# Kernel tuning notes

Hardware: AMD Instinct MI355X
Metric: run time of the kernel (lower is better)

Reference implementation:

```python
import jax, jax.numpy as jnp
import numpy as np

N_TOKENS = 50257  # vocab size (init kwarg)


def setup_inputs() -> dict:
    key = jax.random.key(0)
    # [batch, seq] int token ids in [0, N_TOKENS)
    inputs = jax.random.randint(key, (1024, 512), 0, N_TOKENS, dtype=jnp.int32)
    return {"inputs": inputs}


def reference(inputs) -> jnp.ndarray:
    # Faithful math: sum_j one_hot(inputs[b, j], N_TOKENS) -> token count histogram,
    # then drop token id 0 (padding). Implemented as a scatter-add instead of
    # materializing the [B, S, V] one-hot tensor.
    B, S = inputs.shape
    rows = jnp.arange(B, dtype=jnp.int32)[:, None]  # [B, 1] broadcast against [B, S]
    counts = jnp.zeros((B, N_TOKENS), dtype=jnp.float32)
    counts = counts.at[rows, inputs].add(jnp.float32(1.0))  # [B, V]
    return counts[:, 1:]  # drop token id 0, matches [:, 1:] in the original
```

## Files before the change

kernel.cpp:

```cpp
#include <hip/hip_runtime.h>


#define BATCH 1024
#define SEQ 512
#define VOCAB 50257
#define OUT_COLS (VOCAB - 1)
#define CHUNK 4096
#define NCHUNK 13
#define BLOCK 256

#define LDS_BAR()                                              \
    do {                                                       \
        asm volatile("s_waitcnt lgkmcnt(0)" ::: "memory");     \
        __builtin_amdgcn_s_barrier();                          \
        asm volatile("" ::: "memory");                         \
    } while (0)

__global__ __launch_bounds__(BLOCK) void bow_persistent_kernel(
    const int* __restrict__ tokens, float* __restrict__ out) {
    __shared__ unsigned int hist[CHUNK];

    const int t = threadIdx.x;
    const int b = blockIdx.x >> 1;
    const int h = blockIdx.x & 1;
    const int cbeg = h ? 7 : 0;
    const int cend = h ? NCHUNK : 7;

    const uint4 z4 = make_uint4(0u, 0u, 0u, 0u);
    #pragma unroll
    for (int k = 0; k < 4; ++k)
        *(uint4*)&hist[t * 4 + k * (BLOCK * 4)] = z4;

    const int2 tk = ((const int2*)(tokens + (size_t)b * SEQ))[t];
    const unsigned int cx = (unsigned int)(tk.x - 1);
    const unsigned int cy = (unsigned int)(tk.y - 1);

    LDS_BAR();

    for (int c = cbeg; c < cend; ++c) {
        const unsigned int c0 = (unsigned int)c * CHUNK;

        unsigned int r;
        r = cx - c0;
        if (r < CHUNK) atomicAdd(&hist[r], 1u);
        r = cy - c0;
        if (r < CHUNK) atomicAdd(&hist[r], 1u);

        LDS_BAR();

        uint4 hreg[4];
        #pragma unroll
        for (int k = 0; k < 4; ++k)
            hreg[k] = *(const uint4*)&hist[t * 4 + k * (BLOCK * 4)];
        #pragma unroll
        for (int k = 0; k < 4; ++k)
            *(uint4*)&hist[t * 4 + k * (BLOCK * 4)] = z4;

        LDS_BAR();

        float* orow = out + (size_t)b * OUT_COLS + c0;
        if (c0 + CHUNK <= (unsigned int)OUT_COLS) {
            #pragma unroll
            for (int k = 0; k < 4; ++k) {
                float4 v = make_float4((float)hreg[k].x, (float)hreg[k].y,
                                       (float)hreg[k].z, (float)hreg[k].w);
                *(float4*)(orow + t * 4 + k * (BLOCK * 4)) = v;
            }
        } else {
            const int ncols = OUT_COLS - (int)c0;
            #pragma unroll
            for (int k = 0; k < 4; ++k) {
                const int i = t * 4 + k * (BLOCK * 4);
                if (i < ncols) {
                    float4 v = make_float4((float)hreg[k].x, (float)hreg[k].y,
                                           (float)hreg[k].z, (float)hreg[k].w);
                    *(float4*)(orow + i) = v;
                }
            }
        }
    }
}

extern "C" void kernel_launch(void* const* d_in, const int* in_sizes, int n_in,
                              void* d_out, int out_size, void* d_ws, size_t ws_size,
                              hipStream_t stream) {
    const int* tokens = (const int*)d_in[0];
    float* out = (float*)d_out;

    bow_persistent_kernel<<<dim3(BATCH * 2), dim3(BLOCK), 0, stream>>>(tokens, out);
}
```

Before: 195.3 us.

## Launch one block per row-chunk and skip histogram reads for empty groups

Replaces the persistent kernel, where each block looped over about seven 4096-column chunks, with a 2D grid of 13 x 1024 blocks. Each block handles a single chunk of a single row. This removes the per-chunk barrier and re-zeroing loop and exposes more independent blocks for latency hiding. A small LDS mask records which 4-column groups got any token, so all-zero groups store zeros directly without reading the histogram. In exchange, each row's 2 KB of tokens is re-read by 13 blocks, and there is extra block launch and zeroing overhead per chunk.

New measurement: 194.8 us, median of 2. Within noise of the previous version (-0.3%).

```diff
diff --git a/kernel.cpp b/kernel.cpp
--- a/kernel.cpp
+++ b/kernel.cpp
@@ -6,7 +6,8 @@
 #define VOCAB 50257
 #define OUT_COLS (VOCAB - 1)
 #define CHUNK 4096
-#define NCHUNK 13
+#define NGROUP (CHUNK / 4)
+#define NBLK_PER_ROW 13
 #define BLOCK 256
 
 #define LDS_BAR()                                              \
@@ -16,66 +17,51 @@
         asm volatile("" ::: "memory");                         \
     } while (0)
 
-__global__ __launch_bounds__(BLOCK) void bow_persistent_kernel(
+__global__ __launch_bounds__(BLOCK) void bow_maskstream_kernel(
     const int* __restrict__ tokens, float* __restrict__ out) {
     __shared__ unsigned int hist[CHUNK];
+    __shared__ unsigned int mask[NGROUP];
 
-    const int t = threadIdx.x;
-    const int b = blockIdx.x >> 1;
-    const int h = blockIdx.x & 1;
-    const int cbeg = h ? 7 : 0;
-    const int cend = h ? NCHUNK : 7;
+    const int t  = threadIdx.x;
+    const int c0 = blockIdx.x * CHUNK;
+    const int b  = blockIdx.y;
+
+    const int2 tk = ((const int2*)(tokens + (size_t)b * SEQ))[t];
 
     const uint4 z4 = make_uint4(0u, 0u, 0u, 0u);
     #pragma unroll
     for (int k = 0; k < 4; ++k)
         *(uint4*)&hist[t * 4 + k * (BLOCK * 4)] = z4;
-
-    const int2 tk = ((const int2*)(tokens + (size_t)b * SEQ))[t];
-    const unsigned int cx = (unsigned int)(tk.x - 1);
-    const unsigned int cy = (unsigned int)(tk.y - 1);
+    *(uint4*)&mask[t * 4] = z4;
 
     LDS_BAR();
 
-    for (int c = cbeg; c < cend; ++c) {
-        const unsigned int c0 = (unsigned int)c * CHUNK;
+    unsigned int r;
+    r = (unsigned int)(tk.x - 1 - c0);
+    if (r < CHUNK) { atomicAdd(&hist[r], 1u); mask[r >> 2] = 1u; }
+    r = (unsigned int)(tk.y - 1 - c0);
+    if (r < CHUNK) { atomicAdd(&hist[r], 1u); mask[r >> 2] = 1u; }
 
-        unsigned int r;
-        r = cx - c0;
-        if (r < CHUNK) atomicAdd(&hist[r], 1u);
-        r = cy - c0;
-        if (r < CHUNK) atomicAdd(&hist[r], 1u);
+    LDS_BAR();
 
-        LDS_BAR();
+    float* orow = out + (size_t)b * OUT_COLS + c0;
+    const int ncols = (c0 + CHUNK <= OUT_COLS) ? CHUNK : (OUT_COLS - c0);
 
-        uint4 hreg[4];
-        #pragma unroll
-        for (int k = 0; k < 4; ++k)
-            hreg[k] = *(const uint4*)&hist[t * 4 + k * (BLOCK * 4)];
-        #pragma unroll
-        for (int k = 0; k < 4; ++k)
-            *(uint4*)&hist[t * 4 + k * (BLOCK * 4)] = z4;
+    unsigned int m[4];
+    #pragma unroll
+    for (int k = 0; k < 4; ++k)
+        m[k] = mask[t + k * BLOCK];
 
-        LDS_BAR();
-
-        float* orow = out + (size_t)b * OUT_COLS + c0;
-        if (c0 + CHUNK <= (unsigned int)OUT_COLS) {
-            #pragma unroll
-            for (int k = 0; k < 4; ++k) {
-                float4 v = make_float4((float)hreg[k].x, (float)hreg[k].y,
-                                       (float)hreg[k].z, (float)hreg[k].w);
-                *(float4*)(orow + t * 4 + k * (BLOCK * 4)) = v;
-            }
-        } else {
-            const int ncols = OUT_COLS - (int)c0;
-            #pragma unroll
-            for (int k = 0; k < 4; ++k) {
-                const int i = t * 4 + k * (BLOCK * 4);
-                if (i < ncols) {
-                    float4 v = make_float4((float)hreg[k].x, (float)hreg[k].y,
-                                           (float)hreg[k].z, (float)hreg[k].w);
-                    *(float4*)(orow + i) = v;
-                }
+    #pragma unroll
+    for (int k = 0; k < 4; ++k) {
+        const int base = t * 4 + k * (BLOCK * 4);
+        if (base < ncols) {
+            if (m[k] == 0u) {
+                *(float4*)(orow + base) = make_float4(0.f, 0.f, 0.f, 0.f);
+            } else {
+                const uint4 h = *(const uint4*)&hist[base];
+                *(float4*)(orow + base) = make_float4(
+                    (float)h.x, (float)h.y, (float)h.z, (float)h.w);
             }
         }
     }
@@ -87,5 +73,6 @@
     const int* tokens = (const int*)d_in[0];
     float* out = (float*)d_out;
 
-    bow_persistent_kernel<<<dim3(BATCH * 2), dim3(BLOCK), 0, stream>>>(tokens, out);
+    bow_maskstream_kernel<<<dim3(NBLK_PER_ROW, BATCH), dim3(BLOCK), 0, stream>>>(
+        tokens, out);
 }
```
